# Kernel tuning notes

Hardware: AMD Instinct MI355X
Metric: run time of the kernel (lower is better)

## Reference

```python
import jax, jax.numpy as jnp
import numpy as np

B, S, H = 2, 2048, 1024
NH, HD = 16, 64
WINDOW = 1024
ROPE_THETA = 10000.0
MAX_POS = 2048


def _rope_tables(dtype=jnp.float32):
    # RotaryEmbedding cache: inv_freq over even dims, emb = cat(freqs, freqs)
    inv_freq = 1.0 / (ROPE_THETA ** (jnp.arange(0, HD, 2, dtype=jnp.float32) / HD))
    t = jnp.arange(MAX_POS, dtype=jnp.float32)
    freqs = jnp.einsum('i,j->ij', t, inv_freq)          # [MAX_POS, HD//2]
    emb = jnp.concatenate([freqs, freqs], axis=-1)      # [MAX_POS, HD]
    return jnp.cos(emb).astype(dtype), jnp.sin(emb).astype(dtype)


def _rotate_half(x):
    x1, x2 = x[..., : HD // 2], x[..., HD // 2:]
    return jnp.concatenate([-x2, x1], axis=-1)


def setup_inputs() -> dict:
    key = jax.random.key(0)
    ks = jax.random.split(key, 5)
    sc = 0.02
    hidden_states = jax.random.normal(ks[0], (B, S, H), dtype=jnp.float32)
    position_ids = jnp.tile(jnp.arange(S, dtype=jnp.int64)[None, :], (B, 1))
    wq = jax.random.normal(ks[1], (H, H), dtype=jnp.float32) * sc
    wk = jax.random.normal(ks[2], (H, H), dtype=jnp.float32) * sc
    wv = jax.random.normal(ks[3], (H, H), dtype=jnp.float32) * sc
    wo = jax.random.normal(ks[4], (H, H), dtype=jnp.float32) * sc
    zeros = jnp.zeros((H,), dtype=jnp.float32)
    return {"hidden_states": hidden_states, "position_ids": position_ids,
            "wq": wq, "bq": zeros, "wk": wk, "bk": zeros,
            "wv": wv, "bv": zeros, "wo": wo, "bo": zeros}


def reference(hidden_states, position_ids, wq, bq, wk, bk, wv, bv, wo, bo):
    b, s, _ = hidden_states.shape
    # projections (nn.Linear: x @ W.T + b), split heads -> [B, NH, S, HD]
    def proj(w, bias):
        y = hidden_states @ w.T + bias
        return y.reshape(b, s, NH, HD).transpose(0, 2, 1, 3)
    q, k, v = proj(wq, bq), proj(wk, bk), proj(wv, bv)

    # RoPE: gather cos/sin at position_ids, broadcast over heads
    cos_t, sin_t = _rope_tables(hidden_states.dtype)
    pos = jnp.clip(position_ids, 0, MAX_POS - 1)
    cos = cos_t[pos][:, None, :, :]   # [B, 1, S, HD]
    sin = sin_t[pos][:, None, :, :]
    q = q * cos + _rotate_half(q) * sin
    k = k * cos + _rotate_half(k) * sin

    # scaled dot-product attention with causal + sliding-window band mask
    scores = jnp.einsum('bhqd,bhkd->bhqk', q, k) / jnp.sqrt(jnp.asarray(HD, hidden_states.dtype))
    i = jnp.arange(s)[:, None]
    j = jnp.arange(s)[None, :]
    allowed = (j <= i) & (i - j < WINDOW)          # banded causal mask [S, S]
    neg = jnp.asarray(jnp.finfo(hidden_states.dtype).min, hidden_states.dtype)
    scores = jnp.where(allowed[None, None, :, :], scores, neg)
    probs = jax.nn.softmax(scores, axis=-1)
    ctx = jnp.einsum('bhqk,bhkd->bhqd', probs, v)  # [B, NH, S, HD]
    ctx = ctx.transpose(0, 2, 1, 3).reshape(b, s, H)
    return ctx @ wo.T + bo
```

## Files before the change

kernel.cpp:

```cpp
#include <hip/hip_runtime.h>

#define BATCH 2
#define SDIM 2048
#define HDIM 1024
#define NHEADS 16
#define HEADD 64
#define WIN 1024

typedef __bf16 bf16x8 __attribute__((ext_vector_type(8)));
typedef __bf16 bf16x4 __attribute__((ext_vector_type(4)));
typedef float f32x4 __attribute__((ext_vector_type(4)));
typedef unsigned short u16x8 __attribute__((ext_vector_type(8)));

__device__ __forceinline__ unsigned short bf16_rne(float f) {
    union { float f; unsigned u; } x; x.f = f;
    unsigned r = x.u + 0x7fffu + ((x.u >> 16) & 1u);
    return (unsigned short)(r >> 16);
}

__device__ __forceinline__ void gload_lds16(const unsigned short* g, unsigned short* l) {
    __builtin_amdgcn_global_load_lds(
        (const __attribute__((address_space(1))) void*)g,
        (__attribute__((address_space(3))) void*)l, 16, 0, 0);
}

__global__ __launch_bounds__(256) void prep_kernel(
    const float* __restrict__ hs, const float* __restrict__ wq, const float* __restrict__ wk,
    const float* __restrict__ wv, const float* __restrict__ wo,
    unsigned short* __restrict__ Xb, unsigned short* __restrict__ Wqkv,
    unsigned short* __restrict__ Wob, float2* __restrict__ cstab)
{
    int i = blockIdx.x * 256 + threadIdx.x;
    if (i < 2097152) {
        const float* src; unsigned short* dst; int off;
        if (i < 1048576)      { src = hs; dst = Xb;             off = i; }
        else if (i < 1310720) { src = wq; dst = Wqkv;           off = i - 1048576; }
        else if (i < 1572864) { src = wk; dst = Wqkv + 1048576; off = i - 1310720; }
        else if (i < 1835008) { src = wv; dst = Wqkv + 2097152; off = i - 1572864; }
        else                  { src = wo; dst = Wob;            off = i - 1835008; }
        float4 v = reinterpret_cast<const float4*>(src)[off];
        ushort4 r;
        r.x = bf16_rne(v.x); r.y = bf16_rne(v.y); r.z = bf16_rne(v.z); r.w = bf16_rne(v.w);
        reinterpret_cast<ushort4*>(dst)[off] = r;
    } else {
        int j = i - 2097152;
        int p = j >> 5, f = j & 31;
        float inv = (float)pow(10000.0, -(double)f / 32.0);
        float ang = (float)p * inv;
        cstab[j] = make_float2(cosf(ang), sinf(ang));
    }
}

__global__ __launch_bounds__(256) void gemm_qkv_kernel(
    const unsigned short* __restrict__ Xb,
    const unsigned short* __restrict__ Wb,
    const float* __restrict__ bq, const float* __restrict__ bk, const float* __restrict__ bv,
    const float2* __restrict__ cstab,
    unsigned short* __restrict__ qbuf, unsigned short* __restrict__ kbuf, unsigned short* __restrict__ vbuf)
{
    const int K = 1024;
    const int BUF = 128 * 32;
    __shared__ __align__(16) unsigned short smem[4 * 128 * 32];
    unsigned short* lA = smem;
    unsigned short* lB = smem + 2 * BUF;
    int tid = threadIdx.x;
    int lane = tid & 63, wid = tid >> 6;
    int wm = wid >> 1, wn = wid & 1;
    int lane15 = lane & 15, lhi = lane >> 4;
    int bid = blockIdx.x;
    int xcd = bid & 7, j5 = bid >> 3;
    int m0 = (xcd * 4 + (j5 & 3)) * 128;
    int n0 = (j5 >> 2) * 128;
    int lrow = lane >> 2;
    int swz = (lane & 3) ^ ((lane >> 3) & 3);
    const unsigned short* ga0 = Xb + (long)(m0 + wid * 32      + lrow) * K + swz * 8;
    const unsigned short* ga1 = Xb + (long)(m0 + wid * 32 + 16 + lrow) * K + swz * 8;
    const unsigned short* gb0 = Wb + (long)(n0 + wid * 32      + lrow) * K + swz * 8;
    const unsigned short* gb1 = Wb + (long)(n0 + wid * 32 + 16 + lrow) * K + swz * 8;
    unsigned short* la0 = lA + (wid * 32)      * 32;
    unsigned short* la1 = lA + (wid * 32 + 16) * 32;
    unsigned short* lb0 = lB + (wid * 32)      * 32;
    unsigned short* lb1 = lB + (wid * 32 + 16) * 32;
    int ru = (lhi ^ ((lane15 >> 1) & 3)) * 8;

    f32x4 acc[4][4];
    #pragma unroll
    for (int i = 0; i < 4; i++)
        #pragma unroll
        for (int j = 0; j < 4; j++)
            acc[i][j] = (f32x4){0.f, 0.f, 0.f, 0.f};

#define STAGE_Q(boff, kt) \
    gload_lds16(ga0 + (kt) * 32, la0 + (boff)); \
    gload_lds16(ga1 + (kt) * 32, la1 + (boff)); \
    gload_lds16(gb0 + (kt) * 32, lb0 + (boff)); \
    gload_lds16(gb1 + (kt) * 32, lb1 + (boff));

#define COMPUTE_Q(off) { \
    bf16x8 af[4], bfr[4]; \
    _Pragma("unroll") \
    for (int f = 0; f < 4; f++) { \
        af[f]  = *(const bf16x8*)&lA[(off) + (wm * 64 + f * 16 + lane15) * 32 + ru]; \
        bfr[f] = *(const bf16x8*)&lB[(off) + (wn * 64 + f * 16 + lane15) * 32 + ru]; \
    } \
    _Pragma("unroll") \
    for (int i = 0; i < 4; i++) \
        _Pragma("unroll") \
        for (int j = 0; j < 4; j++) \
            acc[i][j] = __builtin_amdgcn_mfma_f32_16x16x32_bf16(af[i], bfr[j], acc[i][j], 0, 0, 0); \
}

#define WAITQ(n) \
    asm volatile("s_waitcnt vmcnt(" #n ")" ::: "memory"); \
    __builtin_amdgcn_s_barrier(); \
    asm volatile("" ::: "memory");

    STAGE_Q(0, 0);
    STAGE_Q(BUF, 1);
    #pragma unroll 1
    for (int t = 0; t < 30; t += 2) {
        WAITQ(4);
        COMPUTE_Q(0);
        __builtin_amdgcn_s_barrier();
        STAGE_Q(0, t + 2);
        WAITQ(4);
        COMPUTE_Q(BUF);
        __builtin_amdgcn_s_barrier();
        STAGE_Q(BUF, t + 3);
    }
    WAITQ(4);
    COMPUTE_Q(0);
    WAITQ(0);
    COMPUTE_Q(BUF);

#undef STAGE_Q
#undef COMPUTE_Q
#undef WAITQ

    int proj = n0 >> 10;
    int ncol0 = (n0 & 1023) + wn * 64;
    int h = ncol0 >> 6;
    int bb = m0 >> 11, s0r = m0 & (SDIM - 1);
    if (proj == 2) {
        const float* bias = bv;
        __syncthreads();
        #pragma unroll
        for (int fm = 0; fm < 4; fm++)
            #pragma unroll
            for (int reg = 0; reg < 4; reg++) {
                int sl = wm * 64 + fm * 16 + lhi * 4 + reg;
                #pragma unroll
                for (int fn = 0; fn < 4; fn++) {
                    int dl = wn * 64 + fn * 16 + lane15;
                    float v = acc[fm][fn][reg] + bias[(n0 & 1023) + dl];
                    smem[dl * 128 + (sl ^ ((dl & 7) * 8))] = bf16_rne(v);
                }
            }
        __syncthreads();
        int h0 = (n0 & 1023) >> 6;
        #pragma unroll
        for (int it = 0; it < 8; it++) {
            int d = it * 16 + (tid >> 4);
            int s8 = tid & 15;
            u16x8 valv = *(const u16x8*)&smem[d * 128 + ((s8 ^ (d & 7)) * 8)];
            int hh = h0 + (d >> 6);
            *(u16x8*)&vbuf[((long)(bb * NHEADS + hh) * HEADD + (d & 63)) * SDIM + s0r + s8 * 8] = valv;
        }
    } else {
        unsigned short* dst = proj == 0 ? qbuf : kbuf;
        const float* bias = proj == 0 ? bq : bk;
        #pragma unroll
        for (int fm = 0; fm < 4; fm++) {
            #pragma unroll
            for (int reg = 0; reg < 4; reg++) {
                int m = m0 + wm * 64 + fm * 16 + lhi * 4 + reg;
                int s = m & (SDIM - 1);
                long base = ((long)(bb * NHEADS + h) * SDIM + s) * HEADD;
                #pragma unroll
                for (int fn = 0; fn < 2; fn++) {
                    int j = fn * 16 + lane15;
                    float lo = acc[fm][fn][reg]     + bias[ncol0 + j];
                    float hi = acc[fm][fn + 2][reg] + bias[ncol0 + 32 + j];
                    float2 cs = cstab[s * 32 + j];
                    float rl = lo * cs.x - hi * cs.y;
                    float rh = hi * cs.x + lo * cs.y;
                    if (proj == 0) { rl *= 0.125f; rh *= 0.125f; }
                    dst[base + j]      = bf16_rne(rl);
                    dst[base + 32 + j] = bf16_rne(rh);
                }
            }
        }
    }
}

__global__ __launch_bounds__(512) void attn_kernel(
    const unsigned short* __restrict__ qb,
    const unsigned short* __restrict__ kbf,
    const unsigned short* __restrict__ vtb,
    unsigned short* __restrict__ ctxb)
{
    __shared__ __align__(16) unsigned short Kl[64 * 72];
    __shared__ __align__(16) unsigned short Vl[64 * 72];
    __shared__ __align__(16) unsigned short Pl[8][16 * 72];
    int tid = threadIdx.x, lane = tid & 63, wid = tid >> 6;
    int lane15 = lane & 15, lhi = lane >> 4;

    int slot = blockIdx.x;
    int xcd = slot & 7;
    int pos = slot >> 3;
    int hb32 = xcd + 8 * (pos >> 4);
    int h = hb32 & 15, b = hb32 >> 4;
    int qt = 15 - (pos & 15);
    int q0b = qt * 128;
    int qw = q0b + wid * 16;

    long hb = (long)(b * NHEADS + h) * SDIM * HEADD;
    const unsigned short* qptr = qb + hb;
    const unsigned short* kptr = kbf + hb;
    const unsigned short* vt   = vtb + hb;
    unsigned short* Pw = Pl[wid];

    bf16x8 aq0 = *(const bf16x8*)&qptr[(qw + lane15) * HEADD + lhi * 8];
    bf16x8 aq1 = *(const bf16x8*)&qptr[(qw + lane15) * HEADD + 32 + lhi * 8];

    f32x4 acc[4];
    #pragma unroll
    for (int f = 0; f < 4; f++) acc[f] = (f32x4){0.f, 0.f, 0.f, 0.f};
    float rs = 0.f;

    int t0 = q0b - (WIN - 1);
    int kb0 = t0 > 0 ? (t0 >> 6) : 0;
    int kbl = (q0b + 127) >> 6;
    int srow = tid >> 3;
    int sc = (tid & 7) * 8;

    u16x8 kr = *(const u16x8*)&kptr[(kb0 * 64 + srow) * HEADD + sc];
    u16x8 vr = *(const u16x8*)&vt[(long)srow * SDIM + kb0 * 64 + sc];

    for (int kblk = kb0; kblk <= kbl; kblk++) {
        int kbase = kblk * 64;
        __syncthreads();
        *(u16x8*)&Kl[srow * 72 + sc] = kr;
        *(u16x8*)&Vl[srow * 72 + sc] = vr;
        __syncthreads();
        if (kblk < kbl) {
            int nb = (kblk + 1) * 64;
            kr = *(const u16x8*)&kptr[(nb + srow) * HEADD + sc];
            vr = *(const u16x8*)&vt[(long)srow * SDIM + nb + sc];
        }
        if (kbase + 63 < qw - (WIN - 1)) continue;
        if (kbase > qw + 15) continue;

        bool full = (kbase + 63 <= qw) && (qw + 15 - kbase < WIN);
        f32x4 S[4];
        __builtin_amdgcn_s_setprio(1);
        #pragma unroll
        for (int fk = 0; fk < 4; fk++) {
            bf16x8 bk0 = *(const bf16x8*)&Kl[(fk * 16 + lane15) * 72 + lhi * 8];
            bf16x8 bk1 = *(const bf16x8*)&Kl[(fk * 16 + lane15) * 72 + 32 + lhi * 8];
            f32x4 s = (f32x4){0.f, 0.f, 0.f, 0.f};
            s = __builtin_amdgcn_mfma_f32_16x16x32_bf16(bk0, aq0, s, 0, 0, 0);
            s = __builtin_amdgcn_mfma_f32_16x16x32_bf16(bk1, aq1, s, 0, 0, 0);
            S[fk] = s;
        }
        __builtin_amdgcn_s_setprio(0);
        if (!full) {
            int q = qw + lane15;
            #pragma unroll
            for (int fk = 0; fk < 4; fk++)
                #pragma unroll
                for (int r = 0; r < 4; r++) {
                    int k = kbase + fk * 16 + lhi * 4 + r;
                    bool ok = (k <= q) && (q - k < WIN);
                    if (!ok) S[fk][r] = -1e30f;
                }
        }
        #pragma unroll
        for (int fk = 0; fk < 4; fk++) {
            bf16x4 c;
            #pragma unroll
            for (int r = 0; r < 4; r++) {
                float p = __expf(S[fk][r]);
                rs += p;
                c[r] = (__bf16)p;
            }
            *(bf16x4*)&Pw[lane15 * 72 + fk * 16 + lhi * 4] = c;
        }
        __builtin_amdgcn_s_setprio(1);
        #pragma unroll
        for (int ks = 0; ks < 2; ks++) {
            bf16x8 pa = *(const bf16x8*)&Pw[lane15 * 72 + ks * 32 + lhi * 8];
            #pragma unroll
            for (int fd = 0; fd < 4; fd++) {
                bf16x8 bv2 = *(const bf16x8*)&Vl[(fd * 16 + lane15) * 72 + ks * 32 + lhi * 8];
                acc[fd] = __builtin_amdgcn_mfma_f32_16x16x32_bf16(pa, bv2, acc[fd], 0, 0, 0);
            }
        }
        __builtin_amdgcn_s_setprio(0);
    }
    rs += __shfl_xor(rs, 16);
    rs += __shfl_xor(rs, 32);
    float linv[4];
    #pragma unroll
    for (int r = 0; r < 4; r++)
        linv[r] = 1.0f / __shfl(rs, lhi * 4 + r);
    #pragma unroll
    for (int fd = 0; fd < 4; fd++)
        #pragma unroll
        for (int r = 0; r < 4; r++) {
            int q = qw + lhi * 4 + r;
            int d = fd * 16 + lane15;
            ctxb[(((long)b * SDIM + q) * NHEADS + h) * HEADD + d] = bf16_rne(acc[fd][r] * linv[r]);
        }
}

__global__ __launch_bounds__(256) void gemm_o_kernel(
    const unsigned short* __restrict__ Ab,
    const unsigned short* __restrict__ Wb,
    const float* __restrict__ bo,
    float* __restrict__ out)
{
    const int K = 1024;
    const int ABUF = 64 * 32;
    const int BBUF = 128 * 32;
    __shared__ __align__(16) unsigned short lA[3 * ABUF];
    __shared__ __align__(16) unsigned short lB[3 * BBUF];
    int tid = threadIdx.x;
    int lane = tid & 63, wid = tid >> 6;
    int wm = wid >> 1, wn = wid & 1;
    int lane15 = lane & 15, lhi = lane >> 4;
    int bid = blockIdx.x;
    int xcd = bid & 7, j6 = bid >> 3;
    int m0 = (xcd * 8 + (j6 & 7)) * 64;
    int n0 = (j6 >> 3) * 128;
    int lrow = lane >> 2;
    int swz = (lane & 3) ^ ((lane >> 3) & 3);
    const unsigned short* ga0 = Ab + (long)(m0 + wid * 16      + lrow) * K + swz * 8;
    const unsigned short* gb0 = Wb + (long)(n0 + wid * 32      + lrow) * K + swz * 8;
    const unsigned short* gb1 = Wb + (long)(n0 + wid * 32 + 16 + lrow) * K + swz * 8;
    unsigned short* la0 = lA + (wid * 16)      * 32;
    unsigned short* lb0 = lB + (wid * 32)      * 32;
    unsigned short* lb1 = lB + (wid * 32 + 16) * 32;
    int ru = (lhi ^ ((lane15 >> 1) & 3)) * 8;

    f32x4 acc[2][4];
    #pragma unroll
    for (int i = 0; i < 2; i++)
        #pragma unroll
        for (int j = 0; j < 4; j++)
            acc[i][j] = (f32x4){0.f, 0.f, 0.f, 0.f};

#define STAGE_O(aoff, boff, kt) \
    gload_lds16(ga0 + (kt) * 32, la0 + (aoff)); \
    gload_lds16(gb0 + (kt) * 32, lb0 + (boff)); \
    gload_lds16(gb1 + (kt) * 32, lb1 + (boff));

#define COMPUTE_O(aoff, boff) { \
    bf16x8 af[2], bfr[4]; \
    _Pragma("unroll") \
    for (int f = 0; f < 2; f++) \
        af[f]  = *(const bf16x8*)&lA[(aoff) + (wm * 32 + f * 16 + lane15) * 32 + ru]; \
    _Pragma("unroll") \
    for (int f = 0; f < 4; f++) \
        bfr[f] = *(const bf16x8*)&lB[(boff) + (wn * 64 + f * 16 + lane15) * 32 + ru]; \
    _Pragma("unroll") \
    for (int i = 0; i < 2; i++) \
        _Pragma("unroll") \
        for (int j = 0; j < 4; j++) \
            acc[i][j] = __builtin_amdgcn_mfma_f32_16x16x32_bf16(af[i], bfr[j], acc[i][j], 0, 0, 0); \
}

#define WAITO(n) \
    asm volatile("s_waitcnt vmcnt(" #n ")" ::: "memory"); \
    __builtin_amdgcn_s_barrier(); \
    asm volatile("" ::: "memory");

    STAGE_O(0, 0, 0);
    STAGE_O(ABUF, BBUF, 1);
    #pragma unroll 1
    for (int t = 0; t < 30; t += 3) {
        WAITO(3);
        STAGE_O(2 * ABUF, 2 * BBUF, t + 2);
        COMPUTE_O(0, 0);
        WAITO(3);
        STAGE_O(0, 0, t + 3);
        COMPUTE_O(ABUF, BBUF);
        WAITO(3);
        STAGE_O(ABUF, BBUF, t + 4);
        COMPUTE_O(2 * ABUF, 2 * BBUF);
    }
    WAITO(3);
    COMPUTE_O(0, 0);
    WAITO(0);
    COMPUTE_O(ABUF, BBUF);

#undef STAGE_O
#undef COMPUTE_O
#undef WAITO

    #pragma unroll
    for (int fm = 0; fm < 2; fm++)
        #pragma unroll
        for (int reg = 0; reg < 4; reg++) {
            int m = m0 + wm * 32 + fm * 16 + lhi * 4 + reg;
            #pragma unroll
            for (int fn = 0; fn < 4; fn++) {
                int n = n0 + wn * 64 + fn * 16 + lane15;
                out[(long)m * HDIM + n] = acc[fm][fn][reg] + bo[n];
            }
        }
}

extern "C" void kernel_launch(void* const* d_in, const int* in_sizes, int n_in,
                              void* d_out, int out_size, void* d_ws, size_t ws_size,
                              hipStream_t stream) {
    const float* hs = (const float*)d_in[0];
    const float* wq = (const float*)d_in[2];
    const float* bq = (const float*)d_in[3];
    const float* wk = (const float*)d_in[4];
    const float* bk = (const float*)d_in[5];
    const float* wv = (const float*)d_in[6];
    const float* bv = (const float*)d_in[7];
    const float* wo = (const float*)d_in[8];
    const float* bo = (const float*)d_in[9];
    float* out = (float*)d_out;

    char* ws = (char*)d_ws;
    unsigned short* Xb    = (unsigned short*)(ws);
    unsigned short* Wqkv  = (unsigned short*)(ws + (8l  << 20));
    unsigned short* Wob   = (unsigned short*)(ws + (14l << 20));
    float2*         cstab = (float2*)        (ws + (16l << 20));
    unsigned short* qbuf  = (unsigned short*)(ws + (17l << 20));
    unsigned short* kbuf  = (unsigned short*)(ws + (25l << 20));
    unsigned short* vbuf  = (unsigned short*)(ws + (33l << 20));
    unsigned short* ctxb  = (unsigned short*)(ws + (41l << 20));

    prep_kernel<<<8448, 256, 0, stream>>>(hs, wq, wk, wv, wo, Xb, Wqkv, Wob, cstab);
    gemm_qkv_kernel<<<768, 256, 0, stream>>>(Xb, Wqkv, bq, bk, bv, cstab, qbuf, kbuf, vbuf);
    attn_kernel<<<512, 512, 0, stream>>>(qbuf, kbuf, vbuf, ctxb);
    gemm_o_kernel<<<512, 256, 0, stream>>>(ctxb, Wob, bo, out);
}
```

Before: 98.14 us.

## Double-buffer K/V tiles in attention to use one barrier per iteration

The attention kernel's K and V shared-memory tiles become double buffers. While the current tile is computed, the next tile is written into the other buffer from registers, and the tile after that is prefetched from global memory two blocks ahead. This replaces the two __syncthreads per key block with a single lgkmcnt wait plus s_barrier, cutting synchronisation stalls. The cost is twice the K/V LDS footprint, which can lower occupancy. The prologue also always loads block kb0+1, which relies on the window always spanning at least two key blocks.

Measured after the change: 98.85 us. No clear change (+0.7%).

```diff
diff --git a/kernel.cpp b/kernel.cpp
--- a/kernel.cpp
+++ b/kernel.cpp
@@ -199,8 +199,8 @@
     const unsigned short* __restrict__ vtb,
     unsigned short* __restrict__ ctxb)
 {
-    __shared__ __align__(16) unsigned short Kl[64 * 72];
-    __shared__ __align__(16) unsigned short Vl[64 * 72];
+    __shared__ __align__(16) unsigned short Kl[2][64 * 72];
+    __shared__ __align__(16) unsigned short Vl[2][64 * 72];
     __shared__ __align__(16) unsigned short Pl[8][16 * 72];
     int tid = threadIdx.x, lane = tid & 63, wid = tid >> 6;
     int lane15 = lane & 15, lhi = lane >> 4;
@@ -236,67 +236,78 @@
 
     u16x8 kr = *(const u16x8*)&kptr[(kb0 * 64 + srow) * HEADD + sc];
     u16x8 vr = *(const u16x8*)&vt[(long)srow * SDIM + kb0 * 64 + sc];
+    *(u16x8*)&Kl[0][srow * 72 + sc] = kr;
+    *(u16x8*)&Vl[0][srow * 72 + sc] = vr;
+    kr = *(const u16x8*)&kptr[((kb0 + 1) * 64 + srow) * HEADD + sc];
+    vr = *(const u16x8*)&vt[(long)srow * SDIM + (kb0 + 1) * 64 + sc];
+    asm volatile("s_waitcnt lgkmcnt(0)" ::: "memory");
+    __builtin_amdgcn_s_barrier();
+    asm volatile("" ::: "memory");
 
     for (int kblk = kb0; kblk <= kbl; kblk++) {
+        int p = (kblk - kb0) & 1;
         int kbase = kblk * 64;
-        __syncthreads();
-        *(u16x8*)&Kl[srow * 72 + sc] = kr;
-        *(u16x8*)&Vl[srow * 72 + sc] = vr;
-        __syncthreads();
         if (kblk < kbl) {
-            int nb = (kblk + 1) * 64;
+            *(u16x8*)&Kl[p ^ 1][srow * 72 + sc] = kr;
+            *(u16x8*)&Vl[p ^ 1][srow * 72 + sc] = vr;
+        }
+        if (kblk + 2 <= kbl) {
+            int nb = (kblk + 2) * 64;
             kr = *(const u16x8*)&kptr[(nb + srow) * HEADD + sc];
             vr = *(const u16x8*)&vt[(long)srow * SDIM + nb + sc];
         }
-        if (kbase + 63 < qw - (WIN - 1)) continue;
-        if (kbase > qw + 15) continue;
-
-        bool full = (kbase + 63 <= qw) && (qw + 15 - kbase < WIN);
-        f32x4 S[4];
-        __builtin_amdgcn_s_setprio(1);
-        #pragma unroll
-        for (int fk = 0; fk < 4; fk++) {
-            bf16x8 bk0 = *(const bf16x8*)&Kl[(fk * 16 + lane15) * 72 + lhi * 8];
-            bf16x8 bk1 = *(const bf16x8*)&Kl[(fk * 16 + lane15) * 72 + 32 + lhi * 8];
-            f32x4 s = (f32x4){0.f, 0.f, 0.f, 0.f};
-            s = __builtin_amdgcn_mfma_f32_16x16x32_bf16(bk0, aq0, s, 0, 0, 0);
-            s = __builtin_amdgcn_mfma_f32_16x16x32_bf16(bk1, aq1, s, 0, 0, 0);
-            S[fk] = s;
-        }
-        __builtin_amdgcn_s_setprio(0);
-        if (!full) {
-            int q = qw + lane15;
-            #pragma unroll
-            for (int fk = 0; fk < 4; fk++)
+        bool active = !(kbase + 63 < qw - (WIN - 1)) && !(kbase > qw + 15);
+        if (active) {
+            bool full = (kbase + 63 <= qw) && (qw + 15 - kbase < WIN);
+            f32x4 S[4];
+            __builtin_amdgcn_s_setprio(1);
+            #pragma unroll
+            for (int fk = 0; fk < 4; fk++) {
+                bf16x8 bk0 = *(const bf16x8*)&Kl[p][(fk * 16 + lane15) * 72 + lhi * 8];
+                bf16x8 bk1 = *(const bf16x8*)&Kl[p][(fk * 16 + lane15) * 72 + 32 + lhi * 8];
+                f32x4 s = (f32x4){0.f, 0.f, 0.f, 0.f};
+                s = __builtin_amdgcn_mfma_f32_16x16x32_bf16(bk0, aq0, s, 0, 0, 0);
+                s = __builtin_amdgcn_mfma_f32_16x16x32_bf16(bk1, aq1, s, 0, 0, 0);
+                S[fk] = s;
+            }
+            __builtin_amdgcn_s_setprio(0);
+            if (!full) {
+                int q = qw + lane15;
+                #pragma unroll
+                for (int fk = 0; fk < 4; fk++)
+                    #pragma unroll
+                    for (int r = 0; r < 4; r++) {
+                        int k = kbase + fk * 16 + lhi * 4 + r;
+                        bool ok = (k <= q) && (q - k < WIN);
+                        if (!ok) S[fk][r] = -1e30f;
+                    }
+            }
+            #pragma unroll
+            for (int fk = 0; fk < 4; fk++) {
+                bf16x4 c;
                 #pragma unroll
                 for (int r = 0; r < 4; r++) {
-                    int k = kbase + fk * 16 + lhi * 4 + r;
-                    bool ok = (k <= q) && (q - k < WIN);
-                    if (!ok) S[fk][r] = -1e30f;
+                    float pv = __expf(S[fk][r]);
+                    rs += pv;
+                    c[r] = (__bf16)pv;
                 }
-        }
-        #pragma unroll
-        for (int fk = 0; fk < 4; fk++) {
-            bf16x4 c;
-            #pragma unroll
-            for (int r = 0; r < 4; r++) {
-                float p = __expf(S[fk][r]);
-                rs += p;
-                c[r] = (__bf16)p;
-            }
-            *(bf16x4*)&Pw[lane15 * 72 + fk * 16 + lhi * 4] = c;
-        }
-        __builtin_amdgcn_s_setprio(1);
-        #pragma unroll
-        for (int ks = 0; ks < 2; ks++) {
-            bf16x8 pa = *(const bf16x8*)&Pw[lane15 * 72 + ks * 32 + lhi * 8];
-            #pragma unroll
-            for (int fd = 0; fd < 4; fd++) {
-                bf16x8 bv2 = *(const bf16x8*)&Vl[(fd * 16 + lane15) * 72 + ks * 32 + lhi * 8];
-                acc[fd] = __builtin_amdgcn_mfma_f32_16x16x32_bf16(pa, bv2, acc[fd], 0, 0, 0);
-            }
-        }
-        __builtin_amdgcn_s_setprio(0);
+                *(bf16x4*)&Pw[lane15 * 72 + fk * 16 + lhi * 4] = c;
+            }
+            __builtin_amdgcn_s_setprio(1);
+            #pragma unroll
+            for (int ks = 0; ks < 2; ks++) {
+                bf16x8 pa = *(const bf16x8*)&Pw[lane15 * 72 + ks * 32 + lhi * 8];
+                #pragma unroll
+                for (int fd = 0; fd < 4; fd++) {
+                    bf16x8 bv2 = *(const bf16x8*)&Vl[p][(fd * 16 + lane15) * 72 + ks * 32 + lhi * 8];
+                    acc[fd] = __builtin_amdgcn_mfma_f32_16x16x32_bf16(pa, bv2, acc[fd], 0, 0, 0);
+                }
+            }
+            __builtin_amdgcn_s_setprio(0);
+        }
+        asm volatile("s_waitcnt lgkmcnt(0)" ::: "memory");
+        __builtin_amdgcn_s_barrier();
+        asm volatile("" ::: "memory");
     }
     rs += __shfl_xor(rs, 16);
     rs += __shfl_xor(rs, 32);
```
